# Performance work log

Hardware: AMD Instinct MI355X
Metric: run time of the kernel (lower is better)

The kernel has to match this reference:

```python
import jax, jax.numpy as jnp
import numpy as np

NEG_INF = -1.0e7


def positional_encodings(max_seq_len, hidden_size):
    pos = jnp.arange(max_seq_len, dtype=jnp.float32)[:, None]
    dim = jnp.arange(hidden_size // 2, dtype=jnp.float32)[None, :]
    args = pos / (10000.0 ** (2.0 * dim / hidden_size))  # (max_seq_len, h/2)
    pe = jnp.zeros((max_seq_len, hidden_size), dtype=jnp.float32)
    pe = pe.at[:, 0::2].set(jnp.sin(args)).at[:, 1::2].set(jnp.cos(args))
    return pe


def _attention(x_q, x_kv, Wq, bq, Wk, bk, Wv, bv, scale, causal):
    # Linear layers (torch Linear: y = x @ W^T + b; here W stored as (in, out)).
    q = x_q @ Wq + bq            # (B, Sq, H)
    k = x_kv @ Wk + bk           # (B, Sk, H)
    v = x_kv @ Wv + bv           # (B, Sk, H)
    scores = jnp.einsum('bqh,bkh->bqk', q, k) * scale  # (B, Sq, Sk)
    if causal:
        sq, sk = scores.shape[1], scores.shape[2]
        # original adds neg_inf * tril(ones, diag=-1) on (B, Sk, Sq): masked when k_idx > q_idx
        mask = (jnp.arange(sk)[None, :] > jnp.arange(sq)[:, None]).astype(scores.dtype)
        scores = scores + NEG_INF * mask
    w = jax.nn.softmax(scores, axis=-1)                # (B, Sq, Sk)
    ctx = jnp.einsum('bqk,bkh->bqh', w, v)
    return ctx, jnp.transpose(w, (0, 2, 1))            # weights returned as (B, Sk, Sq)


def setup_inputs() -> dict:
    B, S_dec, S_enc, H, V, L = 8, 512, 512, 1024, 32000, 6
    key = jax.random.key(0)
    ks = jax.random.split(key, 20)
    s = 0.02
    inp = {
        'inputs': jax.random.randint(ks[0], (B, S_dec), 0, V),
        'annotations': jax.random.normal(ks[1], (B, S_enc, H), dtype=jnp.float32),
        'hidden_init': jnp.zeros((B, H), dtype=jnp.float32),
        'embedding': jax.random.normal(ks[2], (V, H), dtype=jnp.float32) * s,
        'Wq_s': jax.random.normal(ks[3], (L, H, H), dtype=jnp.float32) * s,
        'bq_s': jnp.zeros((L, H), dtype=jnp.float32),
        'Wk_s': jax.random.normal(ks[4], (L, H, H), dtype=jnp.float32) * s,
        'bk_s': jnp.zeros((L, H), dtype=jnp.float32),
        'Wv_s': jax.random.normal(ks[5], (L, H, H), dtype=jnp.float32) * s,
        'bv_s': jnp.zeros((L, H), dtype=jnp.float32),
        'Wq_c': jax.random.normal(ks[6], (L, H, H), dtype=jnp.float32) * s,
        'bq_c': jnp.zeros((L, H), dtype=jnp.float32),
        'Wk_c': jax.random.normal(ks[7], (L, H, H), dtype=jnp.float32) * s,
        'bk_c': jnp.zeros((L, H), dtype=jnp.float32),
        'Wv_c': jax.random.normal(ks[8], (L, H, H), dtype=jnp.float32) * s,
        'bv_c': jnp.zeros((L, H), dtype=jnp.float32),
        'Wm': jax.random.normal(ks[9], (L, H, H), dtype=jnp.float32) * s,
        'bm': jnp.zeros((L, H), dtype=jnp.float32),
        'Wout': jax.random.normal(ks[10], (H, V), dtype=jnp.float32) * s,
        'bout': jnp.zeros((V,), dtype=jnp.float32),
    }
    return inp


def reference(inputs, annotations, hidden_init, embedding,
              Wq_s, bq_s, Wk_s, bk_s, Wv_s, bv_s,
              Wq_c, bq_c, Wk_c, bk_c, Wv_c, bv_c,
              Wm, bm, Wout, bout):
    B, S = inputs.shape
    L, H, _ = Wq_s.shape
    scale = 1.0 / jnp.sqrt(jnp.asarray(H, dtype=jnp.float32))
    pe = positional_encodings(1000, H)
    contexts = embedding[inputs] + pe[:S]              # (B, S, H)
    enc_ws, self_ws = [], []
    for i in range(L):
        new_ctx, sw = _attention(contexts, contexts,
                                 Wq_s[i], bq_s[i], Wk_s[i], bk_s[i], Wv_s[i], bv_s[i],
                                 scale, causal=True)
        residual = contexts + new_ctx
        new_ctx, ew = _attention(residual, annotations,
                                 Wq_c[i], bq_c[i], Wk_c[i], bk_c[i], Wv_c[i], bv_c[i],
                                 scale, causal=False)
        residual = residual + new_ctx
        mlp = jax.nn.relu(residual @ Wm[i] + bm[i])
        contexts = residual + mlp
        enc_ws.append(ew)
        self_ws.append(sw)
    output = contexts @ Wout + bout                    # (B, S, V)
    return output, (jnp.stack(enc_ws), jnp.stack(self_ws))
```

## Files before the change

### kernel.cpp

```cpp
#include <hip/hip_runtime.h>

typedef __attribute__((ext_vector_type(4))) float f4;
typedef __attribute__((ext_vector_type(8))) short s8v;
typedef __attribute__((ext_vector_type(4))) short s4v;

__device__ __forceinline__ short f2bf(float f) {
  union { float f; unsigned int u; } v; v.f = f;
  unsigned int u = v.u;
  unsigned int r = 0x7fffu + ((u >> 16) & 1u);
  return (short)((u + r) >> 16);
}

__device__ __forceinline__ void glds16(const void* g, void* l) {
  __builtin_amdgcn_global_load_lds((const __attribute__((address_space(1))) void*)g,
                                   (__attribute__((address_space(3))) void*)l, 16, 0, 0);
}

template<int BIAS, int RES, int RELU, int OF32, int OBF, int VT>
__global__ __launch_bounds__(256) void gemmp(
    const unsigned short* __restrict__ A, const unsigned short* __restrict__ Bt,
    const float* __restrict__ bias, const float* __restrict__ bias2,
    const float* __restrict__ res,
    float* __restrict__ Cf, unsigned short* __restrict__ Cb,
    unsigned short* __restrict__ Cvt, int vtoff, int ldvt,
    int lda, int ldb, int ldc, int ldcb, int ldr, int nk,
    long sA, long sB, long sC, long sCb, long sR, long sBias, long sVt) {
  __shared__ __align__(1024) char lds[98304];
  int tid = threadIdx.x;
  int bx = blockIdx.x, by = blockIdx.y, bz = blockIdx.z;
  int bm0 = by * 128, bn0 = bx * 128;
  const char* Ag = (const char*)(A + bz * sA);
  const char* Bg = (const char*)(Bt + bz * sB);
  if (BIAS) bias += bz * sBias;
  int w = tid >> 6, lane = tid & 63;
  int sr = tid >> 3;
  int skb = ((tid & 7) ^ (sr & 7)) << 4;
  size_t la2 = (size_t)lda * 2, lb2 = (size_t)ldb * 2;
  char* bf0 = lds;
  char* bf1 = lds + 32768;
  char* bf2 = lds + 65536;
  int wm = (w >> 1) * 64, wn = (w & 1) * 64;
  int rb = lane & 15;
  int kx = (lane & 7) << 4;
  int kb0 = (lane >> 4) << 4;
  f4 acc[4][4] = {};

  auto stageH = [&](char* buf, int kt, int h) {
    size_t ka = (size_t)kt * 128 + skb;
    if (h == 0) {
      glds16(Ag + (size_t)(bm0 + sr) * la2 + ka,            buf + w * 1024);
      glds16(Ag + (size_t)(bm0 + 32 + sr) * la2 + ka,       buf + 4096 + w * 1024);
      glds16(Bg + (size_t)(bn0 + sr) * lb2 + ka,            buf + 16384 + w * 1024);
      glds16(Bg + (size_t)(bn0 + 32 + sr) * lb2 + ka,       buf + 20480 + w * 1024);
    } else {
      glds16(Ag + (size_t)(bm0 + 64 + sr) * la2 + ka,       buf + 8192 + w * 1024);
      glds16(Ag + (size_t)(bm0 + 96 + sr) * la2 + ka,       buf + 12288 + w * 1024);
      glds16(Bg + (size_t)(bn0 + 64 + sr) * lb2 + ka,       buf + 24576 + w * 1024);
      glds16(Bg + (size_t)(bn0 + 96 + sr) * lb2 + ka,       buf + 28672 + w * 1024);
    }
  };
  auto phase = [&](const char* buf, int ks) {
    const char* Ar = buf + (wm + rb) * 128;
    const char* Br = buf + 16384 + (wn + rb) * 128;
    int kb = (kb0 + ks * 64) ^ kx;
    s8v a[4], b[4];
#pragma unroll
    for (int i = 0; i < 4; ++i) a[i] = *(const s8v*)(Ar + i * 2048 + kb);
#pragma unroll
    for (int j = 0; j < 4; ++j) b[j] = *(const s8v*)(Br + j * 2048 + kb);
    __builtin_amdgcn_s_setprio(1);
#pragma unroll
    for (int i = 0; i < 4; ++i)
#pragma unroll
      for (int j = 0; j < 4; ++j)
        acc[i][j] = __builtin_amdgcn_mfma_f32_16x16x32_bf16(b[j], a[i], acc[i][j], 0, 0, 0);
    __builtin_amdgcn_s_setprio(0);
  };

  stageH(bf0, 0, 0); stageH(bf0, 0, 1);
  stageH(bf1, 1, 0); stageH(bf1, 1, 1);

  for (int t = 0; t < nk - 2; ++t) {
    stageH(bf2, t + 2, 0);
    asm volatile("s_waitcnt vmcnt(12)" ::: "memory");
    __builtin_amdgcn_s_barrier();
    __builtin_amdgcn_sched_barrier(0);
    phase(bf0, 0);
    __builtin_amdgcn_s_barrier();
    stageH(bf2, t + 2, 1);
    __builtin_amdgcn_s_barrier();
    __builtin_amdgcn_sched_barrier(0);
    phase(bf0, 1);
    __builtin_amdgcn_s_barrier();
    char* tp = bf0; bf0 = bf1; bf1 = bf2; bf2 = tp;
  }
  asm volatile("s_waitcnt vmcnt(8)" ::: "memory");
  __builtin_amdgcn_s_barrier();
  __builtin_amdgcn_sched_barrier(0);
  phase(bf0, 0);
  __builtin_amdgcn_s_barrier();
  __builtin_amdgcn_sched_barrier(0);
  phase(bf0, 1);
  __builtin_amdgcn_s_barrier();
  asm volatile("s_waitcnt vmcnt(0)" ::: "memory");
  __builtin_amdgcn_s_barrier();
  __builtin_amdgcn_sched_barrier(0);
  phase(bf1, 0);
  phase(bf1, 1);

  __syncthreads();
  if (VT && bn0 >= vtoff) {
    float* Et = (float*)lds;
#pragma unroll
    for (int i = 0; i < 4; ++i) {
      int lr = wm + i * 16 + (lane & 15);
#pragma unroll
      for (int j = 0; j < 4; ++j) {
        int col0 = wn + j * 16 + ((lane >> 4) << 2);
#pragma unroll
        for (int c = 0; c < 4; ++c) Et[(col0 + c) * 132 + lr] = acc[i][j][c];
      }
    }
    __syncthreads();
    unsigned short* Vp = Cvt + bz * sVt;
    int hb = bn0 - vtoff;
#pragma unroll
    for (int p = 0; p < 16; ++p) {
      int fi = p * 256 + tid;
      int h = fi >> 5, m4 = (fi & 31) * 4;
      f4 v = *(const f4*)&Et[h * 132 + m4];
      float bb = (BIAS == 1) ? bias[bn0 + h] : 0.f;
      s4v o;
      o[0] = f2bf(v[0] + bb); o[1] = f2bf(v[1] + bb);
      o[2] = f2bf(v[2] + bb); o[3] = f2bf(v[3] + bb);
      *(s4v*)(Vp + (size_t)(hb + h) * ldvt + bm0 + m4) = o;
    }
  } else {
    float* E = (float*)lds;
#pragma unroll
    for (int i = 0; i < 4; ++i) {
      int lr = wm + i * 16 + (lane & 15);
      int sw = (lr & 7) << 2;
#pragma unroll
      for (int j = 0; j < 4; ++j) {
        int col = wn + j * 16 + ((lane >> 4) << 2);
        *(f4*)&E[lr * 128 + (col ^ sw)] = acc[i][j];
      }
    }
    __syncthreads();
    float* Cfp = Cf + bz * sC;
    unsigned short* Cbp = Cb + bz * sCb;
    const float* Rp = res + bz * sR;
#pragma unroll
    for (int p = 0; p < 16; ++p) {
      int fi = p * 256 + tid;
      int row = fi >> 5, c4 = fi & 31;
      f4 v = *(const f4*)&E[row * 128 + ((c4 ^ (row & 7)) << 2)];
      int rr = bm0 + row;
      int col = bn0 + c4 * 4;
      if (BIAS == 1) { v[0] += bias[col]; v[1] += bias[col+1]; v[2] += bias[col+2]; v[3] += bias[col+3]; }
      if (BIAS == 2) { float bb = bias[rr]; v[0] += bb; v[1] += bb; v[2] += bb; v[3] += bb; }
      if (RELU) { v[0]=fmaxf(v[0],0.f); v[1]=fmaxf(v[1],0.f); v[2]=fmaxf(v[2],0.f); v[3]=fmaxf(v[3],0.f); }
      if (RES) { f4 rv = *(const f4*)(Rp + (size_t)rr * ldr + col); v[0]+=rv[0]; v[1]+=rv[1]; v[2]+=rv[2]; v[3]+=rv[3]; }
      if (OF32) *(f4*)(Cfp + (size_t)rr * ldc + col) = v;
      if (OBF) {
        s4v o; o[0]=f2bf(v[0]); o[1]=f2bf(v[1]); o[2]=f2bf(v[2]); o[3]=f2bf(v[3]);
        *(s4v*)(Cbp + (size_t)rr * ldcb + col) = o;
      }
    }
  }
}

template<int RES, int OF32, int OBF>
__global__ __launch_bounds__(256) void gemm64(
    const unsigned short* __restrict__ A, const unsigned short* __restrict__ Bt,
    const float* __restrict__ res,
    float* __restrict__ Cf, unsigned short* __restrict__ Cb,
    int lda, int ldb, int ldc, int ldcb, int ldr, int nk,
    long sA, long sB, long sC, long sCb, long sR) {
  __shared__ __align__(1024) char smem[32768];
  int tid = threadIdx.x;
  int bx = blockIdx.x, by = blockIdx.y, bz = blockIdx.z;
  int bm0 = by * 64, bn0 = bx * 64;
  const char* Ag = (const char*)(A + bz * sA);
  const char* Bg = (const char*)(Bt + bz * sB);
  int w = tid >> 6, lane = tid & 63;
  int sr = tid >> 3;
  int skb = ((tid & 7) ^ (sr & 7)) << 4;
  size_t la2 = (size_t)lda * 2, lb2 = (size_t)ldb * 2;
  char* b0 = smem;
  char* b1 = smem + 16384;
  int wm = (w >> 1) * 32, wn = (w & 1) * 32;
  int rb = lane & 15;
  int kx = (lane & 7) << 4;
  int kb0 = (lane >> 4) << 4;
  f4 acc[2][2] = {};

  auto stage = [&](char* buf, int kt) {
    size_t ka = (size_t)kt * 128 + skb;
    glds16(Ag + (size_t)(bm0 + sr) * la2 + ka,      buf + w * 1024);
    glds16(Ag + (size_t)(bm0 + 32 + sr) * la2 + ka, buf + 4096 + w * 1024);
    glds16(Bg + (size_t)(bn0 + sr) * lb2 + ka,      buf + 8192 + w * 1024);
    glds16(Bg + (size_t)(bn0 + 32 + sr) * lb2 + ka, buf + 12288 + w * 1024);
  };
  auto compute = [&](const char* buf) {
    const char* Ar = buf + (wm + rb) * 128;
    const char* Br = buf + 8192 + (wn + rb) * 128;
#pragma unroll
    for (int ks = 0; ks < 2; ++ks) {
      int kb = (kb0 + ks * 64) ^ kx;
      s8v a[2], b[2];
#pragma unroll
      for (int i = 0; i < 2; ++i) a[i] = *(const s8v*)(Ar + i * 2048 + kb);
#pragma unroll
      for (int j = 0; j < 2; ++j) b[j] = *(const s8v*)(Br + j * 2048 + kb);
      __builtin_amdgcn_s_setprio(1);
#pragma unroll
      for (int i = 0; i < 2; ++i)
#pragma unroll
        for (int j = 0; j < 2; ++j)
          acc[i][j] = __builtin_amdgcn_mfma_f32_16x16x32_bf16(b[j], a[i], acc[i][j], 0, 0, 0);
      __builtin_amdgcn_s_setprio(0);
    }
  };

  stage(b0, 0);
  for (int t = 0; t < nk - 1; ++t) {
    stage(b1, t + 1);
    asm volatile("s_waitcnt vmcnt(4)" ::: "memory");
    __builtin_amdgcn_s_barrier();
    __builtin_amdgcn_sched_barrier(0);
    compute(b0);
    __builtin_amdgcn_s_barrier();
    char* tp = b0; b0 = b1; b1 = tp;
  }
  asm volatile("s_waitcnt vmcnt(0)" ::: "memory");
  __builtin_amdgcn_s_barrier();
  __builtin_amdgcn_sched_barrier(0);
  compute(b0);

  float* Cfp = Cf + bz * sC;
  unsigned short* Cbp = Cb + bz * sCb;
  const float* Rp = res + bz * sR;
  float* E = (float*)smem;
  __syncthreads();
#pragma unroll
  for (int i = 0; i < 2; ++i) {
    int lr = wm + i * 16 + (lane & 15);
    int sw = (lr & 7) << 2;
#pragma unroll
    for (int j = 0; j < 2; ++j) {
      int col = wn + j * 16 + ((lane >> 4) << 2);
      *(f4*)&E[lr * 64 + (col ^ sw)] = acc[i][j];
    }
  }
  __syncthreads();
#pragma unroll
  for (int p = 0; p < 4; ++p) {
    int fi = p * 256 + tid;
    int row = fi >> 4, c4 = fi & 15;
    f4 v = *(const f4*)&E[row * 64 + ((c4 ^ (row & 7)) << 2)];
    int rr = bm0 + row;
    int col = bn0 + c4 * 4;
    if (RES) { f4 rv = *(const f4*)(Rp + (size_t)rr * ldr + col); v[0]+=rv[0]; v[1]+=rv[1]; v[2]+=rv[2]; v[3]+=rv[3]; }
    if (OF32) *(f4*)(Cfp + (size_t)rr * ldc + col) = v;
    if (OBF) {
      s4v o; o[0]=f2bf(v[0]); o[1]=f2bf(v[1]); o[2]=f2bf(v[2]); o[3]=f2bf(v[3]);
      *(s4v*)(Cbp + (size_t)rr * ldcb + col) = o;
    }
  }
}

__global__ __launch_bounds__(512) void gemm_logits(
    const unsigned short* __restrict__ A, const unsigned short* __restrict__ Bt,
    const float* __restrict__ bias, float* __restrict__ C) {
  __shared__ __align__(1024) char lds[81920];
  const int ldc = 32000, nk = 16;
  int tid = threadIdx.x;
  int w = tid >> 6, lane = tid & 63;
  int id = blockIdx.y * 500 + blockIdx.x;
  int k = id & 7, j = id >> 3;
  int by = ((k >> 1) << 2) + (j & 3);
  int bx = (k & 1) * 250 + (j >> 2);
  int bm0 = by * 256, bn0 = bx * 64;
  const size_t ld2 = 2048;
  const char* Ag = (const char*)A;
  const char* Bg = (const char*)Bt;
  int srow = (w << 3) + (lane >> 3);
  size_t ska = (size_t)(((lane & 7) ^ (lane >> 3)) << 4);
  char* bf0 = lds;
  char* bf1 = lds + 40960;
  int wm = (w >> 1) * 64;
  int wn = (w & 1) * 32;
  int rsel = lane & 15;
  int kx = (lane & 7) << 4;
  int kb0 = (lane >> 4) << 4;
  f4 acc[4][2] = {};

  auto stage = [&](char* buf, int kt) {
    size_t ka = (size_t)kt * 128 + ska;
    glds16(Ag + (size_t)(bm0 + srow) * ld2 + ka,       buf + w * 1024);
    glds16(Ag + (size_t)(bm0 + 64 + srow) * ld2 + ka,  buf + 8192 + w * 1024);
    glds16(Ag + (size_t)(bm0 + 128 + srow) * ld2 + ka, buf + 16384 + w * 1024);
    glds16(Ag + (size_t)(bm0 + 192 + srow) * ld2 + ka, buf + 24576 + w * 1024);
    glds16(Bg + (size_t)(bn0 + srow) * ld2 + ka,       buf + 32768 + w * 1024);
  };
  auto phase = [&](const char* buf, int ks) {
    const char* Ab = buf + (wm + rsel) * 128;
    const char* Bb = buf + 32768 + (wn + rsel) * 128;
    int kb = (kb0 + ks * 64) ^ kx;
    s8v a0 = *(const s8v*)(Ab + kb);
    s8v a1 = *(const s8v*)(Ab + 2048 + kb);
    s8v a2 = *(const s8v*)(Ab + 4096 + kb);
    s8v a3 = *(const s8v*)(Ab + 6144 + kb);
    s8v q0 = *(const s8v*)(Bb + kb);
    s8v q1 = *(const s8v*)(Bb + 2048 + kb);
    __builtin_amdgcn_s_setprio(1);
    acc[0][0] = __builtin_amdgcn_mfma_f32_16x16x32_bf16(q0, a0, acc[0][0], 0, 0, 0);
    acc[0][1] = __builtin_amdgcn_mfma_f32_16x16x32_bf16(q1, a0, acc[0][1], 0, 0, 0);
    acc[1][0] = __builtin_amdgcn_mfma_f32_16x16x32_bf16(q0, a1, acc[1][0], 0, 0, 0);
    acc[1][1] = __builtin_amdgcn_mfma_f32_16x16x32_bf16(q1, a1, acc[1][1], 0, 0, 0);
    acc[2][0] = __builtin_amdgcn_mfma_f32_16x16x32_bf16(q0, a2, acc[2][0], 0, 0, 0);
    acc[2][1] = __builtin_amdgcn_mfma_f32_16x16x32_bf16(q1, a2, acc[2][1], 0, 0, 0);
    acc[3][0] = __builtin_amdgcn_mfma_f32_16x16x32_bf16(q0, a3, acc[3][0], 0, 0, 0);
    acc[3][1] = __builtin_amdgcn_mfma_f32_16x16x32_bf16(q1, a3, acc[3][1], 0, 0, 0);
    __builtin_amdgcn_s_setprio(0);
  };

  stage(bf0, 0);
  for (int t = 0; t < nk - 1; ++t) {
    stage(bf1, t + 1);
    asm volatile("s_waitcnt vmcnt(5)" ::: "memory");
    __builtin_amdgcn_s_barrier();
    __builtin_amdgcn_sched_barrier(0);
    phase(bf0, 0);
    phase(bf0, 1);
    __builtin_amdgcn_s_barrier();
    char* tp = bf0; bf0 = bf1; bf1 = tp;
  }
  asm volatile("s_waitcnt vmcnt(0)" ::: "memory");
  __builtin_amdgcn_s_barrier();
  __builtin_amdgcn_sched_barrier(0);
  phase(bf0, 0);
  phase(bf0, 1);

  float* E = (float*)lds;
  __syncthreads();
#pragma unroll
  for (int i = 0; i < 4; ++i) {
    int lr = wm + i * 16 + rsel;
    int sw = (lr & 7) << 2;
#pragma unroll
    for (int j = 0; j < 2; ++j) {
      int col = wn + j * 16 + ((lane >> 4) << 2);
      *(f4*)&E[lr * 64 + (col ^ sw)] = acc[i][j];
    }
  }
  __syncthreads();
#pragma unroll
  for (int p = 0; p < 8; ++p) {
    int fi = p * 512 + tid;
    int row = fi >> 4, c4 = fi & 15;
    f4 v = *(const f4*)&E[row * 64 + ((c4 ^ (row & 7)) << 2)];
    int rr = bm0 + row;
    int col = bn0 + c4 * 4;
    v[0] += bias[col]; v[1] += bias[col+1]; v[2] += bias[col+2]; v[3] += bias[col+3];
    __builtin_nontemporal_store(v, (f4*)(C + (size_t)rr * ldc + col));
  }
}

__device__ __forceinline__ void wtrans_tile(const float* src, unsigned short* dst,
                                            int rows, int cols, int c0, int r0) {
  __shared__ float t[64][65];
  int tx = threadIdx.x & 63, ty = threadIdx.x >> 6;
#pragma unroll
  for (int j = 0; j < 16; ++j) {
    int r = j * 4 + ty;
    t[r][tx] = src[(size_t)(r0 + r) * cols + c0 + tx];
  }
  __syncthreads();
#pragma unroll
  for (int j = 0; j < 16; ++j) {
    int n = j * 4 + ty;
    dst[(size_t)(c0 + n) * rows + r0 + tx] = (unsigned short)f2bf(t[tx][n]);
  }
}

__global__ __launch_bounds__(256) void wtrans_k(const float* __restrict__ src,
                                                unsigned short* __restrict__ dst,
                                                int rows, int cols) {
  wtrans_tile(src, dst, rows, cols, blockIdx.x * 64, blockIdx.y * 64);
}

__global__ __launch_bounds__(256) void wtrans_all_k(
    const float* __restrict__ w0, const float* __restrict__ w1,
    const float* __restrict__ w2, const float* __restrict__ w3,
    const float* __restrict__ w4, const float* __restrict__ w5,
    const float* __restrict__ w6, unsigned short* __restrict__ dst) {
  int z = blockIdx.z;
  int l = z / 7, wi = z % 7;
  const float* src;
  switch (wi) {
    case 0: src = w0; break;
    case 1: src = w1; break;
    case 2: src = w2; break;
    case 3: src = w3; break;
    case 4: src = w4; break;
    case 5: src = w5; break;
    default: src = w6; break;
  }
  src += (size_t)l * 1024 * 1024;
  unsigned short* d = dst + (size_t)z * 1024 * 1024;
  wtrans_tile(src, d, 1024, 1024, blockIdx.x * 64, blockIdx.y * 64);
}

__global__ __launch_bounds__(256) void convbf_k(const float* __restrict__ src,
                                                unsigned short* __restrict__ dst, int n4) {
  int i = blockIdx.x * 256 + threadIdx.x;
  if (i >= n4) return;
  f4 f = ((const f4*)src)[i];
  s4v v;
  v[0] = f2bf(f[0]); v[1] = f2bf(f[1]); v[2] = f2bf(f[2]); v[3] = f2bf(f[3]);
  ((s4v*)dst)[i] = v;
}

__global__ __launch_bounds__(1024) void catb_k(
    const float* __restrict__ bq, const float* __restrict__ bk,
    const float* __restrict__ bv, const float* __restrict__ bkc,
    const float* __restrict__ bvc, float* __restrict__ catb,
    float* __restrict__ catbc) {
  int l = blockIdx.x, t = threadIdx.x;
  size_t o = (size_t)l * 1024 + t;
  catb[(size_t)l * 3072 + t] = bq[o];
  catb[(size_t)l * 3072 + 1024 + t] = bk[o];
  catb[(size_t)l * 3072 + 2048 + t] = bv[o];
  catbc[(size_t)l * 2048 + t] = bkc[o];
  catbc[(size_t)l * 2048 + 1024 + t] = bvc[o];
}

template<int CAUSAL>
__global__ __launch_bounds__(512) void smt_k(const float* __restrict__ Sf,
                                             float* __restrict__ outT,
                                             unsigned short* __restrict__ Wb) {
  __shared__ float T[32][524];
  int b = blockIdx.y;
  int q0 = blockIdx.x * 32;
  int t = threadIdx.x;
  const float* Sp = Sf + ((size_t)b * 512 + q0) * 512;
#pragma unroll
  for (int j = 0; j < 8; ++j) {
    int idx = t + 512 * j;
    int r = idx >> 7, c4 = idx & 127;
    f4 v = *(const f4*)(Sp + (size_t)r * 512 + c4 * 4);
    *(f4*)&T[r][c4 * 4] = v;
  }
  __syncthreads();
  int w = t >> 6, l = t & 63;
  int r = 4 * w + (l >> 4);
  int l16 = l & 15;
  int q = q0 + r;
  const float scale = 0.03125f;
  float v[32];
#pragma unroll
  for (int j = 0; j < 32; ++j) {
    int k = l16 + 16 * j;
    float x = T[r][k] * scale;
    if (CAUSAL && k > q) x += -1.0e7f;
    v[j] = x;
  }
  float m = v[0];
#pragma unroll
  for (int j = 1; j < 32; ++j) m = fmaxf(m, v[j]);
  m = fmaxf(m, __shfl_xor(m, 1)); m = fmaxf(m, __shfl_xor(m, 2));
  m = fmaxf(m, __shfl_xor(m, 4)); m = fmaxf(m, __shfl_xor(m, 8));
  float s = 0.f;
#pragma unroll
  for (int j = 0; j < 32; ++j) { v[j] = __expf(v[j] - m); s += v[j]; }
  s += __shfl_xor(s, 1); s += __shfl_xor(s, 2);
  s += __shfl_xor(s, 4); s += __shfl_xor(s, 8);
  float inv = 1.0f / s;
#pragma unroll
  for (int j = 0; j < 32; ++j) T[r][l16 + 16 * j] = v[j] * inv;
  __syncthreads();
  float* op = outT + (size_t)b * 512 * 512 + q0;
  int ql = t & 31, kb = t >> 5;
#pragma unroll
  for (int i = 0; i < 32; ++i) {
    int k = kb + 16 * i;
    __builtin_nontemporal_store(T[ql][k], &op[(size_t)k * 512 + ql]);
  }
  unsigned short* wp = Wb + ((size_t)b * 512 + q0) * 512;
#pragma unroll
  for (int i = 0; i < 4; ++i) {
    int rr = 4 * w + i;
    const float* row = &T[rr][l * 8];
    s8v o;
#pragma unroll
    for (int j = 0; j < 8; ++j) o[j] = f2bf(row[j]);
    *(s8v*)(wp + (size_t)rr * 512 + l * 8) = o;
  }
}

__global__ __launch_bounds__(256) void embed_pe_k(const int* __restrict__ ids,
                                                  const float* __restrict__ emb,
                                                  float* __restrict__ ctx,
                                                  unsigned short* __restrict__ ctxb) {
  int row = blockIdx.x;
  int s = row & 511;
  int t = threadIdx.x;
  int id = ids[row];
  f4 e = *(const f4*)(emb + (size_t)id * 1024 + t * 4);
  int j0 = 2 * t, j1 = 2 * t + 1;
  float fr0 = powf(10000.0f, -2.0f * (float)j0 / 1024.0f);
  float fr1 = powf(10000.0f, -2.0f * (float)j1 / 1024.0f);
  float s0, c0, s1, c1;
  sincosf((float)s * fr0, &s0, &c0);
  sincosf((float)s * fr1, &s1, &c1);
  f4 o;
  o[0] = e[0] + s0; o[1] = e[1] + c0; o[2] = e[2] + s1; o[3] = e[3] + c1;
  *(f4*)(ctx + (size_t)row * 1024 + t * 4) = o;
  s4v ob;
  ob[0] = f2bf(o[0]); ob[1] = f2bf(o[1]); ob[2] = f2bf(o[2]); ob[3] = f2bf(o[3]);
  *(s4v*)(ctxb + (size_t)row * 1024 + t * 4) = ob;
}

extern "C" void kernel_launch(void* const* d_in, const int* in_sizes, int n_in,
                              void* d_out, int out_size, void* d_ws, size_t ws_size,
                              hipStream_t stream) {
  const int B = 8, S = 512, H = 1024, V = 32000, L = 6;
  const int M = B * S;

  const int* ids = (const int*)d_in[0];
  const float* ann = (const float*)d_in[1];
  const float* emb = (const float*)d_in[3];
  const float* bq_s = (const float*)d_in[5];
  const float* bk_s = (const float*)d_in[7];
  const float* bv_s = (const float*)d_in[9];
  const float* bq_c = (const float*)d_in[11];
  const float* bk_c = (const float*)d_in[13];
  const float* bv_c = (const float*)d_in[15];
  const float* bm = (const float*)d_in[17];
  const float* Wout = (const float*)d_in[18];
  const float* bout = (const float*)d_in[19];
  float* out = (float*)d_out;

  char* ws = (char*)d_ws;
  if (ws_size < ((size_t)164 << 20)) return;
  float* X0 = (float*)ws;
  unsigned short* Xs0 = (unsigned short*)(ws + ((size_t)16 << 20));
  unsigned short* Xs1 = (unsigned short*)(ws + ((size_t)24 << 20));
  unsigned short* QKbf = (unsigned short*)(ws + ((size_t)32 << 20));
  unsigned short* Vtbf = (unsigned short*)(ws + ((size_t)48 << 20));
  float* Sbuf = (float*)(ws + ((size_t)56 << 20));
  unsigned short* Wbf = (unsigned short*)(ws + ((size_t)64 << 20));
  unsigned short* annbf = (unsigned short*)(ws + ((size_t)68 << 20));
  unsigned short* WT = (unsigned short*)(ws + ((size_t)76 << 20));
  float* catb = (float*)(ws + ((size_t)160 << 20));
  float* catbc = (float*)(ws + ((size_t)160 << 20) + (96 << 10));
  unsigned short* KcAll = (unsigned short*)d_out;
  unsigned short* VtcAll = (unsigned short*)((char*)d_out + ((size_t)48 << 20));

  size_t enc_off = (size_t)M * V;
  size_t self_off = enc_off + (size_t)L * B * S * S;

  long sQ = (long)S * H;
  long sS = (long)S * S;
  const size_t WSZ = (size_t)H * H;
  const long sW7 = (long)(7 * WSZ);

  embed_pe_k<<<M, 256, 0, stream>>>(ids, emb, X0, Xs0);
  convbf_k<<<(M * H / 4 + 255) / 256, 256, 0, stream>>>(ann, annbf, M * H / 4);
  catb_k<<<L, 1024, 0, stream>>>(bq_s, bk_s, bv_s, bk_c, bv_c, catb, catbc);
  wtrans_all_k<<<dim3(16, 16, 42), 256, 0, stream>>>(
      (const float*)d_in[4], (const float*)d_in[6], (const float*)d_in[8],
      (const float*)d_in[10], (const float*)d_in[12], (const float*)d_in[14],
      (const float*)d_in[16], WT);
  gemmp<1, 0, 0, 0, 1, 1><<<dim3(16, 32, 6), 256, 0, stream>>>(
      annbf, WT + 4 * WSZ, catbc, nullptr, nullptr,
      nullptr, KcAll, VtcAll, 1024, M,
      H, H, 0, H, 0, 16,
      0, sW7, 0, (long)M * H, 0, 2048, (long)H * M);

  unsigned short* Xa = Xs0;
  unsigned short* Xb = Xs1;

  for (int l = 0; l < L; ++l) {
    size_t bo = (size_t)l * H;
    unsigned short* WTl = WT + (size_t)l * 7 * WSZ;

    gemmp<1, 0, 0, 0, 1, 1><<<dim3(24, 32), 256, 0, stream>>>(
        Xa, WTl, catb + (size_t)l * 3072, nullptr, nullptr,
        nullptr, QKbf, Vtbf, 2048, M,
        H, H, 0, 2048, 0, 16,
        0, 0, 0, 0, 0, 0, 0);
    gemm64<0, 1, 0><<<dim3(8, 8, B), 256, 0, stream>>>(
        QKbf, QKbf + 1024, nullptr, Sbuf, nullptr,
        2048, 2048, S, 0, 0, 16, (long)S * 2048, (long)S * 2048, sS, 0, 0);
    smt_k<1><<<dim3(16, B), 512, 0, stream>>>(
        Sbuf, out + self_off + (size_t)l * B * S * S, Wbf);
    gemm64<1, 1, 1><<<dim3(16, 8, B), 256, 0, stream>>>(
        Wbf, Vtbf, X0, X0, Xb,
        S, M, H, H, H, 8, sS, 512, sQ, sQ, sQ);
    gemmp<1, 0, 0, 0, 1, 0><<<dim3(8, 32), 256, 0, stream>>>(
        Xb, WTl + 3 * WSZ, bq_c + bo, nullptr, nullptr,
        nullptr, QKbf, nullptr, 0, 0,
        H, H, 0, 1024, 0, 16,
        0, 0, 0, 0, 0, 0, 0);
    gemm64<0, 1, 0><<<dim3(8, 8, B), 256, 0, stream>>>(
        QKbf, KcAll + (size_t)l * M * H, nullptr, Sbuf, nullptr,
        1024, 1024, S, 0, 0, 16, (long)S * 1024, (long)S * 1024, sS, 0, 0);
    smt_k<0><<<dim3(16, B), 512, 0, stream>>>(
        Sbuf, out + enc_off + (size_t)l * B * S * S, Wbf);
    gemm64<1, 1, 1><<<dim3(16, 8, B), 256, 0, stream>>>(
        Wbf, VtcAll + (size_t)l * H * M, X0, X0, Xa,
        S, M, H, H, H, 8, sS, 512, sQ, sQ, sQ);
    gemmp<1, 1, 1, 1, 1, 0><<<dim3(8, 32), 256, 0, stream>>>(
        Xa, WTl + 6 * WSZ, bm + bo, nullptr, X0,
        X0, Xb, nullptr, 0, 0,
        H, H, H, H, H, 16,
        0, 0, 0, 0, 0, 0, 0);
    unsigned short* tb = Xa; Xa = Xb; Xb = tb;
  }

  wtrans_k<<<dim3(V / 64, H / 64), 256, 0, stream>>>(Wout, WT, H, V);
  gemm_logits<<<dim3(500, 16), 512, 0, stream>>>(Xa, WT, bout, out);
}
```

Baseline: 1.396 ms.

## Replace triple-buffered half-staged GEMM pipeline with simple double buffering

The GEMM main loop goes from a three-buffer pipeline, with each k-tile staged in two halves between compute phases, to a two-buffer scheme. Each iteration now loads the next full k-tile while computing the current one, with one fewer barrier per iteration. LDS drops from 96KB to 68KB (the epilogue transpose still needs about 68KB), which may allow more blocks per CU. The cost is a shallower prefetch depth, so global-load latency is less hidden.

```diff
diff --git a/kernel.cpp b/kernel.cpp
--- a/kernel.cpp
+++ b/kernel.cpp
@@ -25,7 +25,7 @@
     unsigned short* __restrict__ Cvt, int vtoff, int ldvt,
     int lda, int ldb, int ldc, int ldcb, int ldr, int nk,
     long sA, long sB, long sC, long sCb, long sR, long sBias, long sVt) {
-  __shared__ __align__(1024) char lds[98304];
+  __shared__ __align__(1024) char lds[69632];
   int tid = threadIdx.x;
   int bx = blockIdx.x, by = blockIdx.y, bz = blockIdx.z;
   int bm0 = by * 128, bn0 = bx * 128;
@@ -36,77 +36,60 @@
   int sr = tid >> 3;
   int skb = ((tid & 7) ^ (sr & 7)) << 4;
   size_t la2 = (size_t)lda * 2, lb2 = (size_t)ldb * 2;
-  char* bf0 = lds;
-  char* bf1 = lds + 32768;
-  char* bf2 = lds + 65536;
+  char* b0 = lds;
+  char* b1 = lds + 32768;
   int wm = (w >> 1) * 64, wn = (w & 1) * 64;
   int rb = lane & 15;
   int kx = (lane & 7) << 4;
   int kb0 = (lane >> 4) << 4;
   f4 acc[4][4] = {};
 
-  auto stageH = [&](char* buf, int kt, int h) {
+  auto stage = [&](char* buf, int kt) {
     size_t ka = (size_t)kt * 128 + skb;
-    if (h == 0) {
-      glds16(Ag + (size_t)(bm0 + sr) * la2 + ka,            buf + w * 1024);
-      glds16(Ag + (size_t)(bm0 + 32 + sr) * la2 + ka,       buf + 4096 + w * 1024);
-      glds16(Bg + (size_t)(bn0 + sr) * lb2 + ka,            buf + 16384 + w * 1024);
-      glds16(Bg + (size_t)(bn0 + 32 + sr) * lb2 + ka,       buf + 20480 + w * 1024);
-    } else {
-      glds16(Ag + (size_t)(bm0 + 64 + sr) * la2 + ka,       buf + 8192 + w * 1024);
-      glds16(Ag + (size_t)(bm0 + 96 + sr) * la2 + ka,       buf + 12288 + w * 1024);
-      glds16(Bg + (size_t)(bn0 + 64 + sr) * lb2 + ka,       buf + 24576 + w * 1024);
-      glds16(Bg + (size_t)(bn0 + 96 + sr) * lb2 + ka,       buf + 28672 + w * 1024);
-    }
+    glds16(Ag + (size_t)(bm0 + sr) * la2 + ka,      buf + w * 1024);
+    glds16(Ag + (size_t)(bm0 + 32 + sr) * la2 + ka, buf + 4096 + w * 1024);
+    glds16(Ag + (size_t)(bm0 + 64 + sr) * la2 + ka, buf + 8192 + w * 1024);
+    glds16(Ag + (size_t)(bm0 + 96 + sr) * la2 + ka, buf + 12288 + w * 1024);
+    glds16(Bg + (size_t)(bn0 + sr) * lb2 + ka,      buf + 16384 + w * 1024);
+    glds16(Bg + (size_t)(bn0 + 32 + sr) * lb2 + ka, buf + 20480 + w * 1024);
+    glds16(Bg + (size_t)(bn0 + 64 + sr) * lb2 + ka, buf + 24576 + w * 1024);
+    glds16(Bg + (size_t)(bn0 + 96 + sr) * lb2 + ka, buf + 28672 + w * 1024);
   };
-  auto phase = [&](const char* buf, int ks) {
+  auto compute = [&](const char* buf) {
     const char* Ar = buf + (wm + rb) * 128;
     const char* Br = buf + 16384 + (wn + rb) * 128;
-    int kb = (kb0 + ks * 64) ^ kx;
-    s8v a[4], b[4];
-#pragma unroll
-    for (int i = 0; i < 4; ++i) a[i] = *(const s8v*)(Ar + i * 2048 + kb);
-#pragma unroll
-    for (int j = 0; j < 4; ++j) b[j] = *(const s8v*)(Br + j * 2048 + kb);
-    __builtin_amdgcn_s_setprio(1);
-#pragma unroll
-    for (int i = 0; i < 4; ++i)
-#pragma unroll
-      for (int j = 0; j < 4; ++j)
-        acc[i][j] = __builtin_amdgcn_mfma_f32_16x16x32_bf16(b[j], a[i], acc[i][j], 0, 0, 0);
-    __builtin_amdgcn_s_setprio(0);
+#pragma unroll
+    for (int ks = 0; ks < 2; ++ks) {
+      int kb = (kb0 + ks * 64) ^ kx;
+      s8v a[4], b[4];
+#pragma unroll
+      for (int i = 0; i < 4; ++i) a[i] = *(const s8v*)(Ar + i * 2048 + kb);
+#pragma unroll
+      for (int j = 0; j < 4; ++j) b[j] = *(const s8v*)(Br + j * 2048 + kb);
+      __builtin_amdgcn_s_setprio(1);
+#pragma unroll
+      for (int i = 0; i < 4; ++i)
+#pragma unroll
+        for (int j = 0; j < 4; ++j)
+          acc[i][j] = __builtin_amdgcn_mfma_f32_16x16x32_bf16(b[j], a[i], acc[i][j], 0, 0, 0);
+      __builtin_amdgcn_s_setprio(0);
+    }
   };
 
-  stageH(bf0, 0, 0); stageH(bf0, 0, 1);
-  stageH(bf1, 1, 0); stageH(bf1, 1, 1);
-
-  for (int t = 0; t < nk - 2; ++t) {
-    stageH(bf2, t + 2, 0);
-    asm volatile("s_waitcnt vmcnt(12)" ::: "memory");
+  stage(b0, 0);
+  for (int t = 0; t < nk - 1; ++t) {
+    stage(b1, t + 1);
+    asm volatile("s_waitcnt vmcnt(8)" ::: "memory");
     __builtin_amdgcn_s_barrier();
     __builtin_amdgcn_sched_barrier(0);
-    phase(bf0, 0);
+    compute(b0);
     __builtin_amdgcn_s_barrier();
-    stageH(bf2, t + 2, 1);
-    __builtin_amdgcn_s_barrier();
-    __builtin_amdgcn_sched_barrier(0);
-    phase(bf0, 1);
-    __builtin_amdgcn_s_barrier();
-    char* tp = bf0; bf0 = bf1; bf1 = bf2; bf2 = tp;
-  }
-  asm volatile("s_waitcnt vmcnt(8)" ::: "memory");
-  __builtin_amdgcn_s_barrier();
-  __builtin_amdgcn_sched_barrier(0);
-  phase(bf0, 0);
-  __builtin_amdgcn_s_barrier();
-  __builtin_amdgcn_sched_barrier(0);
-  phase(bf0, 1);
-  __builtin_amdgcn_s_barrier();
+    char* tp = b0; b0 = b1; b1 = tp;
+  }
   asm volatile("s_waitcnt vmcnt(0)" ::: "memory");
   __builtin_amdgcn_s_barrier();
   __builtin_amdgcn_sched_barrier(0);
-  phase(bf1, 0);
-  phase(bf1, 1);
+  compute(b0);
 
   __syncthreads();
   if (VT && bn0 >= vtoff) {
```

Result: faster. 1.341 ms (median of 2 runs) (-3.9%).
